# Optimization experiments

Hardware: AMD Instinct MI355X
Metric: run time of the kernel (lower is better)

Reference implementation:

```python
import jax, jax.numpy as jnp
import numpy as np

DIM = 512
HEADS = 8
EPS = 1e-5


def layer_norm(x, g, b):
    mu = jnp.mean(x, axis=-1, keepdims=True)
    var = jnp.mean(jnp.square(x - mu), axis=-1, keepdims=True)
    return (x - mu) * jax.lax.rsqrt(var + EPS) * g + b


def setup_inputs() -> dict:
    key = jax.random.key(0)
    ks = jax.random.split(key, 8)
    d = DIM
    s = 0.02
    return {
        "x": jax.random.normal(ks[0], (2, d, 64, 64), jnp.float32),
        "ln1_g": jnp.ones((d,), jnp.float32),
        "ln1_b": jnp.zeros((d,), jnp.float32),
        "w_qkv": jax.random.normal(ks[1], (d, 3 * d), jnp.float32) * s,
        "b_qkv": jnp.zeros((3 * d,), jnp.float32),
        "w_proj": jax.random.normal(ks[2], (d, d), jnp.float32) * s,
        "b_proj": jnp.zeros((d,), jnp.float32),
        "ln2_g": jnp.ones((d,), jnp.float32),
        "ln2_b": jnp.zeros((d,), jnp.float32),
        "w_ffn1": jax.random.normal(ks[3], (d, 4 * d), jnp.float32) * s,
        "b_ffn1": jnp.zeros((4 * d,), jnp.float32),
        "w_ffn2": jax.random.normal(ks[4], (4 * d, d), jnp.float32) * s,
        "b_ffn2": jnp.zeros((d,), jnp.float32),
    }


def reference(x, ln1_g, ln1_b, w_qkv, b_qkv, w_proj, b_proj,
              ln2_g, ln2_b, w_ffn1, b_ffn1, w_ffn2, b_ffn2):
    B, C, H, W = x.shape
    hd = C // HEADS
    x_in = x
    t = x.reshape(B, C, H * W).transpose(0, 2, 1)  # [B, N, C]
    h = layer_norm(t, ln1_g, ln1_b)
    qkv = h @ w_qkv + b_qkv  # [B, N, 3C]
    q, k, v = jnp.split(qkv, 3, axis=-1)
    def to_heads(a):
        return a.reshape(B, -1, HEADS, hd).transpose(0, 2, 1, 3)  # [B, h, N, hd]
    q, k, v = to_heads(q), to_heads(k), to_heads(v)
    # NOTE: module scales by 1/sqrt(C), not 1/sqrt(head_dim)
    attn = jnp.einsum('bhqd,bhkd->bhqk', q, k) / jnp.sqrt(jnp.float32(C))
    attn = jax.nn.softmax(attn, axis=-1)
    out = jnp.einsum('bhqk,bhkd->bhqd', attn, v)
    out = out.transpose(0, 2, 1, 3).reshape(B, -1, C)
    out = out @ w_proj + b_proj
    t = t + out
    h2 = layer_norm(t, ln2_g, ln2_b)
    ffn = jax.nn.relu(h2 @ w_ffn1 + b_ffn1) @ w_ffn2 + b_ffn2
    t = t + ffn
    y = t.transpose(0, 2, 1).reshape(B, C, H, W)
    return y + x_in
```

## Files before the change

### kernel.cpp

```cpp
#include <hip/hip_runtime.h>
#include <hip/hip_bf16.h>

typedef __bf16 bf16;
typedef __bf16 bf16x8 __attribute__((ext_vector_type(8)));
typedef __bf16 bf16x4 __attribute__((ext_vector_type(4)));
typedef __bf16 bf16x2 __attribute__((ext_vector_type(2)));
typedef float f32x4 __attribute__((ext_vector_type(4)));
typedef int int4v __attribute__((ext_vector_type(4)));
typedef int int2v __attribute__((ext_vector_type(2)));

#define DEV static __device__ __forceinline__

DEV void gload16(const void* g, void* l) {
    __builtin_amdgcn_global_load_lds(
        (const __attribute__((address_space(1))) void*)g,
        (__attribute__((address_space(3))) void*)l, 16, 0, 0);
}

DEV f32x4 mfma16(bf16x8 a, bf16x8 b, f32x4 c) {
    return __builtin_amdgcn_mfma_f32_16x16x32_bf16(a, b, c, 0, 0, 0);
}

DEV int cvtpk(float lo, float hi) {
    int r;
    asm("v_cvt_pk_bf16_f32 %0, %1, %2" : "=v"(r) : "v"(lo), "v"(hi));
    return r;
}

DEV float rexp2(float x) {
    float r;
    asm("v_exp_f32 %0, %1" : "=v"(r) : "v"(x));
    return r;
}

template <bool HASPO>
__global__ __launch_bounds__(512, 2)
void k_tln(const float* __restrict__ x, const bf16* __restrict__ po,
           const float* __restrict__ gg, const float* __restrict__ bb,
           bf16* __restrict__ h) {
    __shared__ char sm[HASPO ? 69632 : 35840];
    bf16* big = (bf16*)sm;
    float* red = (float*)(sm + 33536);
    float* mures = (float*)(sm + 35584);
    bf16* pob = (bf16*)(sm + 35840);

    int t = threadIdx.x;
    int bid = blockIdx.x;
    int nt = bid & 127, b = bid >> 7;
    int n0 = nt * 32;

    if (HASPO) {
        int rr = t >> 4, cs16 = t & 15;
        const bf16* ps = po + (size_t)(b * 4096 + n0 + rr) * 512 + cs16 * 32;
#pragma unroll
        for (int j = 0; j < 4; j++)
            *(bf16x8*)&pob[rr * 524 + cs16 * 32 + j * 8] =
                *(const bf16x8*)(ps + j * 8);
        __syncthreads();
    }

    int n = t & 31, cg = t >> 5;
    const float* xp = x + (size_t)b * 512 * 4096 +
                      (size_t)(cg * 32) * 4096 + n0 + n;
    float s = 0.f, ss = 0.f;
#pragma unroll
    for (int i = 0; i < 32; i++) {
        float v = xp[(size_t)i * 4096];
        if (HASPO) v += (float)pob[n * 524 + cg * 32 + i];
        s += v;
        ss += v * v;
        big[n * 524 + cg * 32 + i] = (bf16)v;
    }
    s += __shfl_xor(s, 32);
    ss += __shfl_xor(ss, 32);
    int w = t >> 6, l = t & 63;
    if (l < 32) {
        red[(w * 32 + n) * 2] = s;
        red[(w * 32 + n) * 2 + 1] = ss;
    }
    __syncthreads();
    if (t < 32) {
        float ts = 0.f, tss = 0.f;
#pragma unroll
        for (int ww = 0; ww < 8; ww++) {
            ts += red[(ww * 32 + t) * 2];
            tss += red[(ww * 32 + t) * 2 + 1];
        }
        float mu = ts * (1.f / 512.f);
        float var = tss * (1.f / 512.f) - mu * mu;
        mures[t * 2] = mu;
        mures[t * 2 + 1] = rsqrtf(var + 1e-5f);
    }
    __syncthreads();

    int nw = t >> 4, cs = t & 15;
    float mu = mures[nw * 2], rs = mures[nw * 2 + 1];
    bf16* hd = h + (size_t)(b * 4096 + n0 + nw) * 512;
#pragma unroll
    for (int j = 0; j < 4; j++) {
        int c = cs * 8 + j * 128;
        bf16x8 vv = *(const bf16x8*)&big[nw * 524 + c];
        f32x4 g0v = *(const f32x4*)(gg + c);
        f32x4 g1v = *(const f32x4*)(gg + c + 4);
        f32x4 b0v = *(const f32x4*)(bb + c);
        f32x4 b1v = *(const f32x4*)(bb + c + 4);
        bf16x8 o;
#pragma unroll
        for (int k = 0; k < 4; k++) {
            o[k] = (bf16)(((float)vv[k] - mu) * rs * g0v[k] + b0v[k]);
            o[k + 4] = (bf16)(((float)vv[k + 4] - mu) * rs * g1v[k] + b1v[k]);
        }
        *(bf16x8*)(hd + c) = o;
    }
}

__global__ __launch_bounds__(256)
void k_wtall(const float* __restrict__ w0, const float* __restrict__ w1,
             const float* __restrict__ w2, const float* __restrict__ w3,
             bf16* __restrict__ d0, bf16* __restrict__ d1,
             bf16* __restrict__ d2, bf16* __restrict__ d3) {
    __shared__ float tile[32][33];
    int bid = blockIdx.x;
    const float* w;
    bf16* d;
    int K, N, t;
    if (bid < 768)       { w = w0; d = d0; K = 512;  N = 1536; t = bid; }
    else if (bid < 1024) { w = w1; d = d1; K = 512;  N = 512;  t = bid - 768; }
    else if (bid < 2048) { w = w2; d = d2; K = 512;  N = 2048; t = bid - 1024; }
    else                 { w = w3; d = d3; K = 2048; N = 512;  t = bid - 2048; }
    int ntn = N >> 5;
    int kt = t / ntn, ntile = t % ntn;
    int k0 = kt * 32, n0 = ntile * 32;
    int tid = threadIdx.x;
    int nl = tid & 31, kl = tid >> 5;
#pragma unroll
    for (int i = 0; i < 4; i++) {
        int k = kl + i * 8;
        tile[k][nl] = w[(size_t)(k0 + k) * N + n0 + nl];
    }
    __syncthreads();
    int kl2 = tid & 31, nl2 = tid >> 5;
#pragma unroll
    for (int i = 0; i < 4; i++) {
        int n = nl2 + i * 8;
        d[(size_t)(n0 + n) * K + k0 + kl2] = (bf16)tile[kl2][n];
    }
}

template <int MODE, int BN>
__global__ __launch_bounds__(256, BN == 64 ? 3 : 2)
void k_gemm(const bf16* __restrict__ A, const bf16* __restrict__ BT,
            const float* __restrict__ bias, bf16* __restrict__ outb,
            bf16* __restrict__ vtout, const float* __restrict__ xin,
            const bf16* __restrict__ poin, float* __restrict__ yout,
            int M, int N, int K) {
    constexpr int CG = BN / 32;
    constexpr int BSZ = CG * 4096;
    __shared__ char smem[32768 + 2 * BSZ];
    int ntn = N / BN;
    int nwg = gridDim.x;
    int bid = blockIdx.x;
    int cpx = nwg >> 3;
    bid = (bid & 7) * cpx + (bid >> 3);
    int bm = bid / ntn, bn = bid % ntn;
    int m0 = bm * 128, n0 = bn * BN;
    int tid = threadIdx.x;
    int w = tid >> 6, l = tid & 63;
    int wm = w >> 1, wn = w & 1;
    int l15 = l & 15, lg = l >> 4;

    f32x4 acc[4][CG];
#pragma unroll
    for (int i = 0; i < 4; i++)
#pragma unroll
        for (int j = 0; j < CG; j++) acc[i][j] = (f32x4){0.f, 0.f, 0.f, 0.f};

    int srow = tid >> 3, sphys = tid & 7;
    int lrow_a = wm * 64 + l15;
    int lrow_b = wn * (BN / 2) + l15;

#define GEMM_STAGE(k0v, bb)                                                  \
    do {                                                                     \
        _Pragma("unroll") for (int s = 0; s < 4; s++) {                      \
            int row = s * 32 + srow;                                         \
            int k16 = sphys ^ (row & 7);                                     \
            gload16(A + (size_t)(m0 + row) * K + (k0v) + k16 * 8,            \
                    smem + (bb) * 16384 + s * 4096 + tid * 16);              \
        }                                                                    \
        _Pragma("unroll") for (int s = 0; s < CG; s++) {                     \
            int row = s * 32 + srow;                                         \
            int k16 = sphys ^ (row & 7);                                     \
            gload16(BT + (size_t)(n0 + row) * K + (k0v) + k16 * 8,           \
                    smem + 32768 + (bb) * BSZ + s * 4096 + tid * 16);        \
        }                                                                    \
    } while (0)

    int nk = K >> 6;
    GEMM_STAGE(0, 0);
    int cur = 0;
    for (int kt = 0; kt < nk; kt++) {
        if (kt + 1 < nk) {
            GEMM_STAGE((kt + 1) << 6, cur ^ 1);
            if constexpr (BN == 128)
                asm volatile("s_waitcnt vmcnt(8)" ::: "memory");
            else
                asm volatile("s_waitcnt vmcnt(6)" ::: "memory");
        } else {
            asm volatile("s_waitcnt vmcnt(0)" ::: "memory");
        }
        __builtin_amdgcn_s_barrier();
        __builtin_amdgcn_sched_barrier(0);
        const char* pA = smem + cur * 16384;
        const char* pB = smem + 32768 + cur * BSZ;
#pragma unroll
        for (int ks = 0; ks < 2; ks++) {
            bf16x8 af[4], bfr[CG];
#pragma unroll
            for (int rg = 0; rg < 4; rg++) {
                int row = lrow_a + rg * 16;
                af[rg] = *(const bf16x8*)(pA + row * 128 +
                                          (((lg + ks * 4) ^ (row & 7)) << 4));
            }
#pragma unroll
            for (int cg = 0; cg < CG; cg++) {
                int row = lrow_b + cg * 16;
                bfr[cg] = *(const bf16x8*)(pB + row * 128 +
                                           (((lg + ks * 4) ^ (row & 7)) << 4));
            }
#pragma unroll
            for (int rg = 0; rg < 4; rg++)
#pragma unroll
                for (int cg = 0; cg < CG; cg++)
                    acc[rg][cg] = mfma16(af[rg], bfr[cg], acc[rg][cg]);
        }
        __builtin_amdgcn_s_barrier();
        cur ^= 1;
    }
#undef GEMM_STAGE

    if constexpr (MODE == 2) {
        if (n0 >= 1024) {
            char* vl = smem;
#pragma unroll
            for (int cg = 0; cg < CG; cg++) {
                int col = wn * (BN / 2) + cg * 16 + l15;
                float bz = bias[n0 + col];
#pragma unroll
                for (int rg = 0; rg < 4; rg++) {
                    int rowb = wm * 64 + rg * 16 + lg * 4;
                    int2v qq = {cvtpk(acc[rg][cg][0] + bz, acc[rg][cg][1] + bz),
                                cvtpk(acc[rg][cg][2] + bz, acc[rg][cg][3] + bz)};
                    *(int2v*)(vl + col * 272 + rowb * 2) = qq;
                }
            }
            __syncthreads();
            int b = m0 >> 12, nrow0 = m0 & 4095;
            int dl = tid >> 3, c8 = tid & 7;
#pragma unroll
            for (int dd = 0; dd < BN / 32; dd++) {
                int d = dd * 32 + dl;
                int ch = (n0 - 1024) + d;
                bf16* dst = vtout +
                    ((size_t)((b * 8 + (ch >> 6)) * 64 + (ch & 63))) * 4096 + nrow0;
#pragma unroll
                for (int half = 0; half < 2; half++) {
                    int chunk = half * 8 + c8;
                    bf16x8 vv = *(const bf16x8*)(vl + d * 272 + chunk * 16);
                    *(bf16x8*)(dst + chunk * 8) = vv;
                }
            }
            return;
        }
    }

    if constexpr (MODE == 3) {
        float* ts = (float*)smem;
        int b = m0 >> 12, nrow0 = m0 & 4095;
#pragma unroll
        for (int cg = 0; cg < CG; cg++) {
            int lcol = wn * (BN / 2) + cg * 16 + l15;
            float bz = bias[n0 + lcol];
#pragma unroll
            for (int rg = 0; rg < 4; rg++) {
#pragma unroll
                for (int j = 0; j < 4; j++) {
                    int lrow = wm * 64 + rg * 16 + lg * 4 + j;
                    float v = acc[rg][cg][j] + bz +
                        (float)poin[(size_t)(m0 + lrow) * 512 + n0 + lcol];
                    ts[lcol * 132 + lrow] = v;
                }
            }
        }
        __syncthreads();
        int nl = (tid & 31) * 4, chh = tid >> 5;
#pragma unroll
        for (int q = 0; q < 8; q++) {
            int c = chh + q * 8;
            size_t off = ((size_t)b * 512 + n0 + c) * 4096 + nrow0 + nl;
            f32x4 xv = *(const f32x4*)(xin + off);
            f32x4 tv = *(const f32x4*)&ts[c * 132 + nl];
            f32x4 ov;
#pragma unroll
            for (int k2 = 0; k2 < 4; k2++) ov[k2] = 2.f * xv[k2] + tv[k2];
            *(f32x4*)(yout + off) = ov;
        }
        return;
    }

    constexpr int RS = BN * 2 + 8;
    constexpr int CH = BN / 8;
    char* ep = smem;
#pragma unroll
    for (int cg = 0; cg < CG; cg++) {
        int lcol = wn * (BN / 2) + cg * 16 + l15;
        float bz = bias[n0 + lcol];
#pragma unroll
        for (int rg = 0; rg < 4; rg++) {
#pragma unroll
            for (int j = 0; j < 4; j++) {
                int lrow = wm * 64 + rg * 16 + lg * 4 + j;
                float v = acc[rg][cg][j] + bz;
                *(bf16*)(ep + lrow * RS + lcol * 2) = (bf16)v;
            }
        }
    }
    __syncthreads();
    int cch = tid & (CH - 1);
    int rof = tid / CH;
    constexpr int RPP = 256 / CH;
#pragma unroll
    for (int i = 0; i < 128 / RPP; i++) {
        int row = i * RPP + rof;
        bf16x8 vv = *(const bf16x8*)(ep + row * RS + cch * 16);
        *(bf16x8*)(outb + (size_t)(m0 + row) * N + n0 + cch * 8) = vv;
    }
}

__global__ __launch_bounds__(512, 2)
void k_gemm8(const bf16* __restrict__ A, const bf16* __restrict__ BT,
             const float* __restrict__ bias, bf16* __restrict__ outb) {
    __shared__ char sL[131072];
    int bid = blockIdx.x;
    bid = (bid & 7) * 32 + (bid >> 3);
    int bm = bid >> 3, bn = bid & 7;
    int m0 = bm * 256, n0 = bn * 256;
    int tid = threadIdx.x;
    int w = tid >> 6, l = tid & 63;
    int wm = w >> 2, wn = w & 3;
    int l15 = l & 15, lg = l >> 4;
    int cpr = (lg ^ ((l15 >> 1) & 3)) << 4;

    f32x4 acc[8][4];
#pragma unroll
    for (int i = 0; i < 8; i++)
#pragma unroll
        for (int j = 0; j < 4; j++) acc[i][j] = (f32x4){0.f, 0.f, 0.f, 0.f};

    int srow = tid >> 2, scp = tid & 3;
    int kofs = (scp ^ ((srow >> 1) & 3)) * 8;
    const bf16* gA0 = A + (size_t)(m0 + srow) * 512 + kofs;
    const bf16* gA1 = gA0 + 128 * 512;
    const bf16* gB0 = BT + (size_t)(n0 + srow) * 512 + kofs;
    const bf16* gB1 = gB0 + 128 * 512;
    char* dA = sL + tid * 16;
    char* dB = sL + 65536 + tid * 16;
    const char* pA0 = sL + (wm * 128 + l15) * 64 + cpr;
    const char* pB0 = sL + 65536 + (wn * 64 + l15) * 64 + cpr;

#define STGA(T, S, BUF)                                                       \
    gload16(gA0 + (T) * 64 + (S) * 32, dA + (BUF) * 32768 + (S) * 16384);     \
    gload16(gA1 + (T) * 64 + (S) * 32, dA + (BUF) * 32768 + (S) * 16384 + 8192);
#define STGB(T, S, BUF)                                                       \
    gload16(gB0 + (T) * 64 + (S) * 32, dB + (BUF) * 32768 + (S) * 16384);     \
    gload16(gB1 + (T) * 64 + (S) * 32, dB + (BUF) * 32768 + (S) * 16384 + 8192);
#define WB8 asm volatile("s_waitcnt vmcnt(8)" ::: "memory"); __builtin_amdgcn_s_barrier();
#define WB4 asm volatile("s_waitcnt vmcnt(4)" ::: "memory"); __builtin_amdgcn_s_barrier();
#define WB0 asm volatile("s_waitcnt vmcnt(0)" ::: "memory"); __builtin_amdgcn_s_barrier();
#define WBN

    bf16x8 bfr[4];

#define PH(BUF, S, RGH, WAITC, STGC)                                          \
    {                                                                         \
        WAITC                                                                 \
        if ((RGH) == 0) {                                                     \
            _Pragma("unroll") for (int cg = 0; cg < 4; cg++)                  \
                bfr[cg] = *(const bf16x8*)(pB0 + (BUF) * 32768 +              \
                                           (S) * 16384 + cg * 1024);          \
        }                                                                     \
        bf16x8 af[4];                                                         \
        _Pragma("unroll") for (int i = 0; i < 4; i++)                         \
            af[i] = *(const bf16x8*)(pA0 + (BUF) * 32768 + (S) * 16384 +      \
                                     ((RGH) * 4 + i) * 1024);                 \
        STGC                                                                  \
        __builtin_amdgcn_s_barrier();                                         \
        asm volatile("s_waitcnt lgkmcnt(0)" ::: "memory");                    \
        __builtin_amdgcn_sched_barrier(0);                                    \
        __builtin_amdgcn_s_setprio(1);                                        \
        _Pragma("unroll") for (int i = 0; i < 4; i++)                         \
            _Pragma("unroll") for (int cg = 0; cg < 4; cg++)                  \
                acc[(RGH) * 4 + i][cg] =                                      \
                    mfma16(af[i], bfr[cg], acc[(RGH) * 4 + i][cg]);           \
        __builtin_amdgcn_s_setprio(0);                                        \
    }

#define TILEF(T, BUF)                                                         \
    PH(BUF, 0, 0, WB8, STGA(T + 1, 1, BUF ^ 1))                               \
    PH(BUF, 0, 1, WBN, STGB(T + 1, 1, BUF ^ 1))                               \
    PH(BUF, 1, 0, WB8, STGA(T + 2, 0, BUF))                                   \
    PH(BUF, 1, 1, WBN, STGB(T + 2, 0, BUF))

    STGA(0, 0, 0) STGB(0, 0, 0) STGA(0, 1, 0) STGB(0, 1, 0)
    STGA(1, 0, 1) STGB(1, 0, 1)

    TILEF(0, 0) TILEF(1, 1) TILEF(2, 0) TILEF(3, 1) TILEF(4, 0) TILEF(5, 1)
    PH(0, 0, 0, WB8, STGA(7, 1, 1))
    PH(0, 0, 1, WBN, STGB(7, 1, 1))
    PH(0, 1, 0, WB8, )
    PH(0, 1, 1, WBN, )
    PH(1, 0, 0, WB4, )
    PH(1, 0, 1, WBN, )
    PH(1, 1, 0, WB0, )
    PH(1, 1, 1, WBN, )
#undef TILEF
#undef PH
#undef WB8
#undef WB4
#undef WB0
#undef WBN
#undef STGA
#undef STGB

    float bz[4];
#pragma unroll
    for (int cg = 0; cg < 4; cg++) bz[cg] = bias[n0 + wn * 64 + cg * 16 + l15];
#pragma unroll
    for (int h2 = 0; h2 < 2; h2++) {
        __syncthreads();
        if (wm == h2) {
#pragma unroll
            for (int rg = 0; rg < 8; rg++)
#pragma unroll
                for (int cg = 0; cg < 4; cg++)
#pragma unroll
                    for (int j = 0; j < 4; j++) {
                        int rl = rg * 16 + lg * 4 + j;
                        int cl = wn * 64 + cg * 16 + l15;
                        float v = fmaxf(acc[rg][cg][j] + bz[cg], 0.f);
                        *(bf16*)(sL + rl * 520 + cl * 2) = (bf16)v;
                    }
        }
        __syncthreads();
        int cch = tid & 31, rof = tid >> 5;
#pragma unroll
        for (int p = 0; p < 8; p++) {
            int row = p * 16 + rof;
            bf16x8 vv = *(const bf16x8*)(sL + row * 520 + cch * 16);
            *(bf16x8*)(outb + (size_t)(m0 + h2 * 128 + row) * 2048 +
                       n0 + cch * 8) = vv;
        }
    }
}

__global__ __launch_bounds__(512, 4)
void k_attn(const bf16* __restrict__ qkvb, const bf16* __restrict__ vt,
            bf16* __restrict__ attno) {
    __shared__ bf16 sK[2][64 * 64];
    __shared__ bf16 sV[2][64 * 64];
    const float sc = 0.044194173824159216f * 1.4426950408889634f;
    int bid = blockIdx.x;
    int nb = (bid & 7) * 64 + (bid >> 3);
    int bh = nb >> 5, qt = nb & 31;
    int b = bh >> 3, hh = bh & 7;
    int q0 = qt * 128;
    int tid = threadIdx.x, w = tid >> 6, l = tid & 63;
    int l15 = l & 15, lg = l >> 4, l7 = l15 & 7;
    int vperm = ((lg & 1) << 1) | (lg >> 1);
    const bf16* qbase = qkvb + (size_t)b * 4096 * 1536 + hh * 64;
    const bf16* kbase = qbase + 512;
    const bf16* vbase = vt + (size_t)bh * 64 * 4096;
    int srow = tid >> 3, sphys = tid & 7;

    const char* kp0 = (const char*)&sK[0][0] + l15 * 128 + ((lg ^ l7) << 4);
    const char* kp1 = (const char*)&sK[0][0] + l15 * 128 + (((4 + lg) ^ l7) << 4);
    const char* vp0 = (const char*)&sV[0][0] + l15 * 128 + ((vperm ^ l7) << 4);
    const char* vp1 = (const char*)&sV[0][0] + l15 * 128 + (((4 + vperm) ^ l7) << 4);
    char* dK0 = (char*)&sK[0][0] + tid * 16;
    char* dV0 = (char*)&sV[0][0] + tid * 16;
    const char* kg = (const char*)(kbase + srow * 1536 + (sphys ^ (srow & 7)) * 8);
    const char* vg = (const char*)(vbase + srow * 4096 + (sphys ^ (srow & 7)) * 8);

    gload16(kg, dK0);
    gload16(vg, dV0);
    kg += 196608;
    vg += 128;

    bf16x8 qf[2];
#pragma unroll
    for (int ks = 0; ks < 2; ks++) {
        bf16x8 v = *(const bf16x8*)(qbase +
            (size_t)(q0 + w * 16 + l15) * 1536 + ks * 32 + lg * 8);
        bf16x8 o;
#pragma unroll
        for (int j = 0; j < 8; j++) o[j] = (bf16)((float)v[j] * sc);
        qf[ks] = o;
    }
    bf16x8 ones;
#pragma unroll
    for (int j = 0; j < 8; j++) ones[j] = (bf16)1.0f;

    const f32x4 kZ = {0.f, 0.f, 0.f, 0.f};
    f32x4 accl = kZ;
    f32x4 acc[4];
#pragma unroll
    for (int df = 0; df < 4; df++) acc[df] = kZ;

#define ABODY(BUF, PF)                                                        \
    {                                                                         \
        if (PF) {                                                             \
            gload16(kg, dK0 + (1 - (BUF)) * 8192);                            \
            gload16(vg, dV0 + (1 - (BUF)) * 8192);                            \
            kg += 196608;                                                     \
            vg += 128;                                                        \
            asm volatile("s_waitcnt vmcnt(2)" ::: "memory");                  \
        } else {                                                              \
            asm volatile("s_waitcnt vmcnt(0)" ::: "memory");                  \
        }                                                                     \
        __builtin_amdgcn_s_barrier();                                         \
        __builtin_amdgcn_sched_barrier(0);                                    \
        f32x4 s0, s1, s2, s3;                                                 \
        __builtin_amdgcn_s_setprio(1);                                        \
        s0 = mfma16(*(const bf16x8*)(kp0 + (BUF) * 8192 + 0 * 2048), qf[0], kZ); \
        s0 = mfma16(*(const bf16x8*)(kp1 + (BUF) * 8192 + 0 * 2048), qf[1], s0); \
        s1 = mfma16(*(const bf16x8*)(kp0 + (BUF) * 8192 + 1 * 2048), qf[0], kZ); \
        s1 = mfma16(*(const bf16x8*)(kp1 + (BUF) * 8192 + 1 * 2048), qf[1], s1); \
        __builtin_amdgcn_s_setprio(0);                                        \
        float e0 = rexp2(s0[0]), e1 = rexp2(s0[1]);                           \
        float e2 = rexp2(s0[2]), e3 = rexp2(s0[3]);                           \
        float e4 = rexp2(s1[0]), e5 = rexp2(s1[1]);                           \
        float e6 = rexp2(s1[2]), e7 = rexp2(s1[3]);                           \
        __builtin_amdgcn_s_setprio(1);                                        \
        s2 = mfma16(*(const bf16x8*)(kp0 + (BUF) * 8192 + 2 * 2048), qf[0], kZ); \
        s2 = mfma16(*(const bf16x8*)(kp1 + (BUF) * 8192 + 2 * 2048), qf[1], s2); \
        s3 = mfma16(*(const bf16x8*)(kp0 + (BUF) * 8192 + 3 * 2048), qf[0], kZ); \
        s3 = mfma16(*(const bf16x8*)(kp1 + (BUF) * 8192 + 3 * 2048), qf[1], s3); \
        __builtin_amdgcn_s_setprio(0);                                        \
        int p0 = cvtpk(e0, e1), p1 = cvtpk(e2, e3);                           \
        int p2 = cvtpk(e4, e5), p3 = cvtpk(e6, e7);                           \
        asm("v_permlane16_swap_b32 %0, %1" : "+v"(p2), "+v"(p0));             \
        asm("v_permlane16_swap_b32 %0, %1" : "+v"(p3), "+v"(p1));             \
        {                                                                     \
            int4v ai = {p0, p1, p2, p3};                                      \
            bf16x8 af = __builtin_bit_cast(bf16x8, ai);                       \
            __builtin_amdgcn_s_setprio(1);                                    \
            acc[0] = mfma16(af, *(const bf16x8*)(vp0 + (BUF) * 8192 + 0 * 2048), acc[0]); \
            acc[1] = mfma16(af, *(const bf16x8*)(vp0 + (BUF) * 8192 + 1 * 2048), acc[1]); \
            acc[2] = mfma16(af, *(const bf16x8*)(vp0 + (BUF) * 8192 + 2 * 2048), acc[2]); \
            acc[3] = mfma16(af, *(const bf16x8*)(vp0 + (BUF) * 8192 + 3 * 2048), acc[3]); \
            accl = mfma16(af, ones, accl);                                    \
            __builtin_amdgcn_s_setprio(0);                                    \
        }                                                                     \
        float e8 = rexp2(s2[0]), e9 = rexp2(s2[1]);                           \
        float e10 = rexp2(s2[2]), e11 = rexp2(s2[3]);                         \
        float e12 = rexp2(s3[0]), e13 = rexp2(s3[1]);                         \
        float e14 = rexp2(s3[2]), e15 = rexp2(s3[3]);                         \
        int p4 = cvtpk(e8, e9), p5 = cvtpk(e10, e11);                         \
        int p6 = cvtpk(e12, e13), p7 = cvtpk(e14, e15);                       \
        asm("v_permlane16_swap_b32 %0, %1" : "+v"(p6), "+v"(p4));             \
        asm("v_permlane16_swap_b32 %0, %1" : "+v"(p7), "+v"(p5));             \
        {                                                                     \
            int4v ai = {p4, p5, p6, p7};                                      \
            bf16x8 af = __builtin_bit_cast(bf16x8, ai);                       \
            __builtin_amdgcn_s_setprio(1);                                    \
            acc[0] = mfma16(af, *(const bf16x8*)(vp1 + (BUF) * 8192 + 0 * 2048), acc[0]); \
            acc[1] = mfma16(af, *(const bf16x8*)(vp1 + (BUF) * 8192 + 1 * 2048), acc[1]); \
            acc[2] = mfma16(af, *(const bf16x8*)(vp1 + (BUF) * 8192 + 2 * 2048), acc[2]); \
            acc[3] = mfma16(af, *(const bf16x8*)(vp1 + (BUF) * 8192 + 3 * 2048), acc[3]); \
            accl = mfma16(af, ones, accl);                                    \
            __builtin_amdgcn_s_setprio(0);                                    \
        }                                                                     \
        __builtin_amdgcn_s_barrier();                                         \
    }

    for (int tt = 0; tt < 31; tt++) {
        ABODY(0, 1)
        ABODY(1, 1)
    }
    ABODY(0, 1)
    ABODY(1, 0)
#undef ABODY

    float invq[4];
#pragma unroll
    for (int j = 0; j < 4; j++) invq[j] = 1.0f / accl[j];

    bf16* ow = (bf16*)&sK[0][0] + w * 16 * 64;
#pragma unroll
    for (int df = 0; df < 4; df++) {
        int chunk = df * 2 + (l15 >> 3);
        int within = l15 & 7;
#pragma unroll
        for (int j = 0; j < 4; j++) {
            int q = lg * 4 + j;
            *(bf16*)((char*)ow + q * 128 + ((chunk ^ (q & 7)) << 4) + within * 2) =
                (bf16)(acc[df][j] * invq[j]);
        }
    }
    __syncthreads();
    const char* owr = (const char*)ow;
#pragma unroll
    for (int half = 0; half < 2; half++) {
        int r = l >> 2, ch = (l & 3) + half * 4;
        bf16x8 vv = *(const bf16x8*)(owr + r * 128 + ((ch ^ (r & 7)) << 4));
        *(bf16x8*)(attno + (size_t)(b * 4096 + q0 + w * 16 + r) * 512 +
                   hh * 64 + ch * 8) = vv;
    }
}

extern "C" void kernel_launch(void* const* d_in, const int* in_sizes, int n_in,
                              void* d_out, int out_size, void* d_ws, size_t ws_size,
                              hipStream_t stream) {
    const float* x = (const float*)d_in[0];
    const float* ln1g = (const float*)d_in[1];
    const float* ln1b = (const float*)d_in[2];
    const float* wqkv = (const float*)d_in[3];
    const float* bqkv = (const float*)d_in[4];
    const float* wproj = (const float*)d_in[5];
    const float* bproj = (const float*)d_in[6];
    const float* ln2g = (const float*)d_in[7];
    const float* ln2b = (const float*)d_in[8];
    const float* wffn1 = (const float*)d_in[9];
    const float* bffn1 = (const float*)d_in[10];
    const float* wffn2 = (const float*)d_in[11];
    const float* bffn2 = (const float*)d_in[12];
    float* y = (float*)d_out;

    char* ws = (char*)d_ws;
    bf16* po   = (bf16*)(ws + 0);
    bf16* h    = (bf16*)(ws + 16777216);
    bf16* qkvb = (bf16*)(ws + 25165824);
    bf16* vtb  = (bf16*)(ws + 50331648);
    bf16* f1   = (bf16*)(ws + 25165824);
    bf16* wqT  = (bf16*)(ws + 58720256);
    bf16* wpT  = (bf16*)(ws + 60293120);
    bf16* w1T  = (bf16*)(ws + 60817408);
    bf16* w2T  = (bf16*)(ws + 62914560);
    bf16* attno = h;

    k_tln<false><<<256, 512, 0, stream>>>(x, nullptr, ln1g, ln1b, h);
    k_wtall<<<3072, 256, 0, stream>>>(wqkv, wproj, wffn1, wffn2,
                                      wqT, wpT, w1T, w2T);
    k_gemm<2, 128><<<768, 256, 0, stream>>>(h, wqT, bqkv, qkvb, vtb,
                                            nullptr, nullptr, nullptr,
                                            8192, 1536, 512);
    k_attn<<<512, 512, 0, stream>>>(qkvb, vtb, attno);
    k_gemm<0, 64><<<512, 256, 0, stream>>>(attno, wpT, bproj, po, nullptr,
                                           nullptr, nullptr, nullptr,
                                           8192, 512, 512);
    k_tln<true><<<256, 512, 0, stream>>>(x, po, ln2g, ln2b, h);
    k_gemm8<<<256, 512, 0, stream>>>(h, w1T, bffn1, f1);
    k_gemm<3, 64><<<512, 256, 0, stream>>>(f1, w2T, bffn2, nullptr, nullptr,
                                           x, po, y, 8192, 512, 2048);
}
```

Baseline: 172.3 us.

## Software-pipeline attention loop: overlap next QK^T with current softmax and PV

After: 175.9 us. 1.02x slower.

```diff
diff --git a/kernel.cpp b/kernel.cpp
--- a/kernel.cpp
+++ b/kernel.cpp
@@ -490,10 +490,12 @@
     const char* kg = (const char*)(kbase + srow * 1536 + (sphys ^ (srow & 7)) * 8);
     const char* vg = (const char*)(vbase + srow * 4096 + (sphys ^ (srow & 7)) * 8);
 
-    gload16(kg, dK0);
-    gload16(vg, dV0);
-    kg += 196608;
-    vg += 128;
+#define SKST(BUF)                                                             \
+    { gload16(kg, dK0 + (BUF) * 8192); kg += 196608; }
+#define SVST(BUF)                                                             \
+    { gload16(vg, dV0 + (BUF) * 8192); vg += 128; }
+
+    SKST(0) SVST(0) SKST(1) SVST(1)
 
     bf16x8 qf[2];
 #pragma unroll
@@ -514,86 +516,99 @@
     f32x4 acc[4];
 #pragma unroll
     for (int df = 0; df < 4; df++) acc[df] = kZ;
-
-#define ABODY(BUF, PF)                                                        \
+    f32x4 sE0, sE1, sE2, sE3, sO0, sO1, sO2, sO3;
+
+#define QKC(BUFQ, N0, N1, N2, N3)                                             \
+    __builtin_amdgcn_s_setprio(1);                                            \
+    N0 = mfma16(*(const bf16x8*)(kp0 + (BUFQ) * 8192 + 0 * 2048), qf[0], kZ); \
+    N0 = mfma16(*(const bf16x8*)(kp1 + (BUFQ) * 8192 + 0 * 2048), qf[1], N0); \
+    N1 = mfma16(*(const bf16x8*)(kp0 + (BUFQ) * 8192 + 1 * 2048), qf[0], kZ); \
+    N1 = mfma16(*(const bf16x8*)(kp1 + (BUFQ) * 8192 + 1 * 2048), qf[1], N1); \
+    N2 = mfma16(*(const bf16x8*)(kp0 + (BUFQ) * 8192 + 2 * 2048), qf[0], kZ); \
+    N2 = mfma16(*(const bf16x8*)(kp1 + (BUFQ) * 8192 + 2 * 2048), qf[1], N2); \
+    N3 = mfma16(*(const bf16x8*)(kp0 + (BUFQ) * 8192 + 3 * 2048), qf[0], kZ); \
+    N3 = mfma16(*(const bf16x8*)(kp1 + (BUFQ) * 8192 + 3 * 2048), qf[1], N3); \
+    __builtin_amdgcn_s_setprio(0);
+
+#define SOFTPV(BUFP, O0, O1, O2, O3)                                          \
     {                                                                         \
-        if (PF) {                                                             \
-            gload16(kg, dK0 + (1 - (BUF)) * 8192);                            \
-            gload16(vg, dV0 + (1 - (BUF)) * 8192);                            \
-            kg += 196608;                                                     \
-            vg += 128;                                                        \
-            asm volatile("s_waitcnt vmcnt(2)" ::: "memory");                  \
-        } else {                                                              \
-            asm volatile("s_waitcnt vmcnt(0)" ::: "memory");                  \
-        }                                                                     \
-        __builtin_amdgcn_s_barrier();                                         \
-        __builtin_amdgcn_sched_barrier(0);                                    \
-        f32x4 s0, s1, s2, s3;                                                 \
-        __builtin_amdgcn_s_setprio(1);                                        \
-        s0 = mfma16(*(const bf16x8*)(kp0 + (BUF) * 8192 + 0 * 2048), qf[0], kZ); \
-        s0 = mfma16(*(const bf16x8*)(kp1 + (BUF) * 8192 + 0 * 2048), qf[1], s0); \
-        s1 = mfma16(*(const bf16x8*)(kp0 + (BUF) * 8192 + 1 * 2048), qf[0], kZ); \
-        s1 = mfma16(*(const bf16x8*)(kp1 + (BUF) * 8192 + 1 * 2048), qf[1], s1); \
-        __builtin_amdgcn_s_setprio(0);                                        \
-        float e0 = rexp2(s0[0]), e1 = rexp2(s0[1]);                           \
-        float e2 = rexp2(s0[2]), e3 = rexp2(s0[3]);                           \
-        float e4 = rexp2(s1[0]), e5 = rexp2(s1[1]);                           \
-        float e6 = rexp2(s1[2]), e7 = rexp2(s1[3]);                           \
-        __builtin_amdgcn_s_setprio(1);                                        \
-        s2 = mfma16(*(const bf16x8*)(kp0 + (BUF) * 8192 + 2 * 2048), qf[0], kZ); \
-        s2 = mfma16(*(const bf16x8*)(kp1 + (BUF) * 8192 + 2 * 2048), qf[1], s2); \
-        s3 = mfma16(*(const bf16x8*)(kp0 + (BUF) * 8192 + 3 * 2048), qf[0], kZ); \
-        s3 = mfma16(*(const bf16x8*)(kp1 + (BUF) * 8192 + 3 * 2048), qf[1], s3); \
-        __builtin_amdgcn_s_setprio(0);                                        \
+        float e0 = rexp2(O0[0]), e1 = rexp2(O0[1]);                           \
+        float e2 = rexp2(O0[2]), e3 = rexp2(O0[3]);                           \
+        float e4 = rexp2(O1[0]), e5 = rexp2(O1[1]);                           \
+        float e6 = rexp2(O1[2]), e7 = rexp2(O1[3]);                           \
+        float e8 = rexp2(O2[0]), e9 = rexp2(O2[1]);                           \
+        float e10 = rexp2(O2[2]), e11 = rexp2(O2[3]);                         \
+        float e12 = rexp2(O3[0]), e13 = rexp2(O3[1]);                         \
+        float e14 = rexp2(O3[2]), e15 = rexp2(O3[3]);                         \
         int p0 = cvtpk(e0, e1), p1 = cvtpk(e2, e3);                           \
         int p2 = cvtpk(e4, e5), p3 = cvtpk(e6, e7);                           \
+        int p4 = cvtpk(e8, e9), p5 = cvtpk(e10, e11);                         \
+        int p6 = cvtpk(e12, e13), p7 = cvtpk(e14, e15);                       \
         asm("v_permlane16_swap_b32 %0, %1" : "+v"(p2), "+v"(p0));             \
         asm("v_permlane16_swap_b32 %0, %1" : "+v"(p3), "+v"(p1));             \
+        asm("v_permlane16_swap_b32 %0, %1" : "+v"(p6), "+v"(p4));             \
+        asm("v_permlane16_swap_b32 %0, %1" : "+v"(p7), "+v"(p5));             \
         {                                                                     \
             int4v ai = {p0, p1, p2, p3};                                      \
             bf16x8 af = __builtin_bit_cast(bf16x8, ai);                       \
             __builtin_amdgcn_s_setprio(1);                                    \
-            acc[0] = mfma16(af, *(const bf16x8*)(vp0 + (BUF) * 8192 + 0 * 2048), acc[0]); \
-            acc[1] = mfma16(af, *(const bf16x8*)(vp0 + (BUF) * 8192 + 1 * 2048), acc[1]); \
-            acc[2] = mfma16(af, *(const bf16x8*)(vp0 + (BUF) * 8192 + 2 * 2048), acc[2]); \
-            acc[3] = mfma16(af, *(const bf16x8*)(vp0 + (BUF) * 8192 + 3 * 2048), acc[3]); \
+            acc[0] = mfma16(af, *(const bf16x8*)(vp0 + (BUFP) * 8192 + 0 * 2048), acc[0]); \
+            acc[1] = mfma16(af, *(const bf16x8*)(vp0 + (BUFP) * 8192 + 1 * 2048), acc[1]); \
+            acc[2] = mfma16(af, *(const bf16x8*)(vp0 + (BUFP) * 8192 + 2 * 2048), acc[2]); \
+            acc[3] = mfma16(af, *(const bf16x8*)(vp0 + (BUFP) * 8192 + 3 * 2048), acc[3]); \
             accl = mfma16(af, ones, accl);                                    \
             __builtin_amdgcn_s_setprio(0);                                    \
         }                                                                     \
-        float e8 = rexp2(s2[0]), e9 = rexp2(s2[1]);                           \
-        float e10 = rexp2(s2[2]), e11 = rexp2(s2[3]);                         \
-        float e12 = rexp2(s3[0]), e13 = rexp2(s3[1]);                         \
-        float e14 = rexp2(s3[2]), e15 = rexp2(s3[3]);                         \
-        int p4 = cvtpk(e8, e9), p5 = cvtpk(e10, e11);                         \
-        int p6 = cvtpk(e12, e13), p7 = cvtpk(e14, e15);                       \
-        asm("v_permlane16_swap_b32 %0, %1" : "+v"(p6), "+v"(p4));             \
-        asm("v_permlane16_swap_b32 %0, %1" : "+v"(p7), "+v"(p5));             \
         {                                                                     \
             int4v ai = {p4, p5, p6, p7};                                      \
             bf16x8 af = __builtin_bit_cast(bf16x8, ai);                       \
             __builtin_amdgcn_s_setprio(1);                                    \
-            acc[0] = mfma16(af, *(const bf16x8*)(vp1 + (BUF) * 8192 + 0 * 2048), acc[0]); \
-            acc[1] = mfma16(af, *(const bf16x8*)(vp1 + (BUF) * 8192 + 1 * 2048), acc[1]); \
-            acc[2] = mfma16(af, *(const bf16x8*)(vp1 + (BUF) * 8192 + 2 * 2048), acc[2]); \
-            acc[3] = mfma16(af, *(const bf16x8*)(vp1 + (BUF) * 8192 + 3 * 2048), acc[3]); \
+            acc[0] = mfma16(af, *(const bf16x8*)(vp1 + (BUFP) * 8192 + 0 * 2048), acc[0]); \
+            acc[1] = mfma16(af, *(const bf16x8*)(vp1 + (BUFP) * 8192 + 1 * 2048), acc[1]); \
+            acc[2] = mfma16(af, *(const bf16x8*)(vp1 + (BUFP) * 8192 + 2 * 2048), acc[2]); \
+            acc[3] = mfma16(af, *(const bf16x8*)(vp1 + (BUFP) * 8192 + 3 * 2048), acc[3]); \
             accl = mfma16(af, ones, accl);                                    \
             __builtin_amdgcn_s_setprio(0);                                    \
         }                                                                     \
+    }
+
+    asm volatile("s_waitcnt vmcnt(0)" ::: "memory");
+    __builtin_amdgcn_s_barrier();
+    __builtin_amdgcn_sched_barrier(0);
+    QKC(0, sE0, sE1, sE2, sE3)
+
+#define BODY(BUFP, BUFQ, N0, N1, N2, N3, O0, O1, O2, O3, PF)                  \
+    {                                                                         \
+        asm volatile("s_waitcnt vmcnt(1)" ::: "memory");                      \
         __builtin_amdgcn_s_barrier();                                         \
+        __builtin_amdgcn_sched_barrier(0);                                    \
+        if (PF) SKST(BUFP)                                                    \
+        QKC(BUFQ, N0, N1, N2, N3)                                             \
+        SOFTPV(BUFP, O0, O1, O2, O3)                                          \
+        __builtin_amdgcn_s_barrier();                                         \
+        if (PF) SVST(BUFP)                                                    \
     }
 
     for (int tt = 0; tt < 31; tt++) {
-        ABODY(0, 1)
-        ABODY(1, 1)
-    }
-    ABODY(0, 1)
-    ABODY(1, 0)
-#undef ABODY
+        BODY(0, 1, sO0, sO1, sO2, sO3, sE0, sE1, sE2, sE3, 1)
+        BODY(1, 0, sE0, sE1, sE2, sE3, sO0, sO1, sO2, sO3, 1)
+    }
+    BODY(0, 1, sO0, sO1, sO2, sO3, sE0, sE1, sE2, sE3, 0)
+    asm volatile("s_waitcnt vmcnt(0)" ::: "memory");
+    __builtin_amdgcn_s_barrier();
+    __builtin_amdgcn_sched_barrier(0);
+    SOFTPV(1, sO0, sO1, sO2, sO3)
+#undef BODY
+#undef SOFTPV
+#undef QKC
+#undef SKST
+#undef SVST
 
     float invq[4];
 #pragma unroll
     for (int j = 0; j < 4; j++) invq[j] = 1.0f / accl[j];
 
+    __syncthreads();
     bf16* ow = (bf16*)&sK[0][0] + w * 16 * 64;
 #pragma unroll
     for (int df = 0; df < 4; df++) {
```
